# Performance work log

Hardware: AMD Instinct MI355X
Metric: run time of the kernel (lower is better)

The kernel has to match this reference:

```python
import jax, jax.numpy as jnp
import numpy as np

N = 50000   # num nodes
C = 256     # in_channels
O = 256     # out_channels
D = 32      # fixed degree per node
S = 16      # num_samples


def setup_inputs() -> dict:
    key = jax.random.key(0)
    ks = jax.random.split(key, 8)
    w = 1.0 / np.sqrt(C).astype(np.float32)
    x = jax.random.normal(ks[0], (N, C), dtype=jnp.float32)
    neighbors = jax.random.randint(ks[1], (N, D), 0, N)  # padded adjacency (degree D for every node)
    W_self = jax.random.uniform(ks[2], (C, O), dtype=jnp.float32, minval=-w, maxval=w)
    b_self = jax.random.uniform(ks[3], (O,), dtype=jnp.float32, minval=-w, maxval=w)
    W_neigh = jax.random.uniform(ks[4], (C, O), dtype=jnp.float32, minval=-w, maxval=w)
    b_neigh = jax.random.uniform(ks[5], (O,), dtype=jnp.float32, minval=-w, maxval=w)
    W_coarsen = jax.random.uniform(ks[6], (C, O), dtype=jnp.float32, minval=-w, maxval=w)
    b_coarsen = jax.random.uniform(ks[7], (O,), dtype=jnp.float32, minval=-w, maxval=w)
    return dict(x=x, W_self=W_self, b_self=b_self, W_neigh=W_neigh, b_neigh=b_neigh,
                W_coarsen=W_coarsen, b_coarsen=b_coarsen, neighbors=neighbors)


def reference(x, W_self, b_self, W_neigh, b_neigh, W_coarsen, b_coarsen, neighbors):
    # Deterministic partition of each node's D neighbors into S sampled + (D-S) unsampled.
    sampled = neighbors[:, :S]     # [N, S]
    unsampled = neighbors[:, S:]   # [N, D-S]
    # Batched gather + mean aggregation (replaces the per-node Python loop).
    agg_s = jnp.mean(x[sampled], axis=1)    # [N, C]
    agg_u = jnp.mean(x[unsampled], axis=1)  # [N, C]
    # out[v] = W_self x[v] + W_neigh mean(sampled) + W_coarsen mean(unsampled) (+ biases)
    out = (x @ W_self + b_self) + (agg_s @ W_neigh + b_neigh) + (agg_u @ W_coarsen + b_coarsen)
    return out
```

## Files before the change

### kernel.cpp

```cpp
#include <hip/hip_runtime.h>
#include <stdint.h>
#include <stddef.h>


#define NN   50000
#define NPAD 50176
#define ODIM 256
#define NTK  24

typedef __bf16 bf16x8 __attribute__((ext_vector_type(8)));
typedef float  f32x4  __attribute__((ext_vector_type(4)));
typedef float  f32x2  __attribute__((ext_vector_type(2)));
typedef unsigned short u16x8 __attribute__((ext_vector_type(8)));
typedef unsigned short u16x4 __attribute__((ext_vector_type(4)));

static __device__ __forceinline__ unsigned short f2b(float f) {
    unsigned u = __builtin_bit_cast(unsigned, f);
    u += 0x7fffu + ((u >> 16) & 1u);
    return (unsigned short)(u >> 16);
}

__global__ void k_prep_w(const float* __restrict__ Wself, const float* __restrict__ bself,
                         const float* __restrict__ Wneigh, const float* __restrict__ bneigh,
                         const float* __restrict__ Wcoar, const float* __restrict__ bcoar,
                         unsigned short* __restrict__ Wb, float* __restrict__ bias) {
    int k = blockIdx.x;
    int n = threadIdx.x;
    const float* W = (k < 256) ? Wself : (k < 512) ? Wneigh : Wcoar;
    int kl = k & 255;
    float v = W[(size_t)kl * ODIM + n];
    int g = k >> 3;
    int j = k & 7;
    Wb[((size_t)g * ODIM + n) * 8 + j] = f2b(v);
    if (k == 0) bias[n] = bself[n] + bneigh[n] + bcoar[n];
}

__global__ void k_convert_x(const float* __restrict__ x, unsigned short* __restrict__ Ax,
                            unsigned char* __restrict__ X8) {
    int p = blockIdx.x * 256 + threadIdx.x;
    if (p >= NN * 32) return;
    int i  = p >> 5;
    int c8 = p & 31;
    const f32x4* src = (const f32x4*)(x + (size_t)i * 256 + c8 * 8);
    f32x4 v0 = src[0], v1 = src[1];
    u16x8 o;
    o[0] = f2b(v0[0]); o[1] = f2b(v0[1]); o[2] = f2b(v0[2]); o[3] = f2b(v0[3]);
    o[4] = f2b(v1[0]); o[5] = f2b(v1[1]); o[6] = f2b(v1[2]); o[7] = f2b(v1[3]);
    *(u16x8*)(Ax + ((size_t)c8 * NPAD + i) * 8) = o;
    unsigned d0 = __builtin_amdgcn_cvt_pk_fp8_f32(v0[0], v0[1], 0, false);
    d0 = (unsigned)__builtin_amdgcn_cvt_pk_fp8_f32(v0[2], v0[3], d0, true);
    unsigned d1 = __builtin_amdgcn_cvt_pk_fp8_f32(v1[0], v1[1], 0, false);
    d1 = (unsigned)__builtin_amdgcn_cvt_pk_fp8_f32(v1[2], v1[3], d1, true);
    uint2 o8; o8.x = d0; o8.y = d1;
    *(uint2*)(X8 + (size_t)i * 256 + c8 * 8) = o8;
}

__global__ __launch_bounds__(512) void k_gather(const int* __restrict__ nbr,
                                                const unsigned char* __restrict__ X8,
                                                unsigned short* __restrict__ Ax) {
    __shared__ unsigned short aggl[8][512];
    const int wid  = threadIdx.x >> 6;
    const int lane = threadIdx.x & 63;
    const int i = blockIdx.x * 8 + wid;
    const int* nb = nbr + (size_t)i * 32;
    float s0 = 0, s1 = 0, s2 = 0, s3 = 0, u0 = 0, u1 = 0, u2 = 0, u3 = 0;
#pragma unroll
    for (int j = 0; j < 32; ++j) {
        int idx = nb[j];
        unsigned d = *(const unsigned*)(X8 + (size_t)idx * 256 + lane * 4);
        f32x2 lo = __builtin_amdgcn_cvt_pk_f32_fp8(d, false);
        f32x2 hi = __builtin_amdgcn_cvt_pk_f32_fp8(d, true);
        if (j < 16) { s0 += lo[0]; s1 += lo[1]; s2 += hi[0]; s3 += hi[1]; }
        else        { u0 += lo[0]; u1 += lo[1]; u2 += hi[0]; u3 += hi[1]; }
    }
    const float rc = 1.0f / 16.0f;
    u16x4 os = { f2b(s0 * rc), f2b(s1 * rc), f2b(s2 * rc), f2b(s3 * rc) };
    u16x4 ou = { f2b(u0 * rc), f2b(u1 * rc), f2b(u2 * rc), f2b(u3 * rc) };
    *(u16x4*)&aggl[wid][lane * 4]       = os;
    *(u16x4*)&aggl[wid][256 + lane * 4] = ou;
    __syncthreads();
    const int tau = threadIdx.x;
    const int gl = tau >> 3, r = tau & 7;
    u16x8 v = *(const u16x8*)&aggl[r][gl * 8];
    *(u16x8*)(Ax + ((size_t)(32 + gl) * NPAD + blockIdx.x * 8 + r) * 8) = v;
}

__global__ __launch_bounds__(512, 4) void k_gemm(const unsigned short* __restrict__ Ax,
                                                 const unsigned short* __restrict__ Wb,
                                                 const float* __restrict__ bias,
                                                 float* __restrict__ out) {
    __shared__ __align__(16) unsigned short lds[3][12288];
    const int tid  = threadIdx.x;
    const int wid  = tid >> 6;
    const int lane = tid & 63;
    const int l15 = lane & 15, l4 = lane >> 4;
    const int row0 = blockIdx.x * 128;
    const int wr = wid >> 2, wc = wid & 3;

    f32x4 acc[4][4] = {};

    auto stage = [&](int buf, int t) {
#pragma unroll
        for (int i = 0; i < 3; ++i) {
            const int u = wid * 3 + i;
            if (u < 8) {
                const int kc = u >> 1, half = u & 1;
                const int g  = t * 4 + kc;
                const unsigned short* src =
                    Ax + ((size_t)g * NPAD + row0 + half * 64 + lane) * 8;
                unsigned short* dst = &lds[buf][kc * 1024 + half * 512];
                __builtin_amdgcn_global_load_lds(
                    (const __attribute__((address_space(1))) void*)src,
                    (__attribute__((address_space(3))) void*)dst, 16, 0, 0);
            } else {
                const int v = u - 8;
                const int kc = v >> 2, nq = v & 3;
                const int g  = t * 4 + kc;
                const unsigned short* src =
                    Wb + ((size_t)g * ODIM + nq * 64 + lane) * 8;
                unsigned short* dst = &lds[buf][4096 + kc * 2048 + nq * 512];
                __builtin_amdgcn_global_load_lds(
                    (const __attribute__((address_space(1))) void*)src,
                    (__attribute__((address_space(3))) void*)dst, 16, 0, 0);
            }
        }
    };

    stage(0, 0);
    stage(1, 1);
#pragma unroll
    for (int t = 0; t < NTK; ++t) {
        if (t < NTK - 1) asm volatile("s_waitcnt vmcnt(3)" ::: "memory");
        else            asm volatile("s_waitcnt vmcnt(0)" ::: "memory");
        __builtin_amdgcn_s_barrier();
        __builtin_amdgcn_sched_barrier(0);
        if (t + 2 < NTK) stage((t + 2) % 3, t + 2);
        const int buf = t % 3;
        bf16x8 af[4], bfr[4];
#pragma unroll
        for (int mi = 0; mi < 4; ++mi)
            af[mi] = *(const bf16x8*)&lds[buf][l4 * 1024 + (wr * 64 + mi * 16 + l15) * 8];
#pragma unroll
        for (int ni = 0; ni < 4; ++ni)
            bfr[ni] = *(const bf16x8*)&lds[buf][4096 + l4 * 2048 + (wc * 64 + ni * 16 + l15) * 8];
#pragma unroll
        for (int mi = 0; mi < 4; ++mi)
#pragma unroll
            for (int ni = 0; ni < 4; ++ni)
                acc[mi][ni] = __builtin_amdgcn_mfma_f32_16x16x32_bf16(
                    af[mi], bfr[ni], acc[mi][ni], 0, 0, 0);
    }

#pragma unroll
    for (int mi = 0; mi < 4; ++mi) {
        const int row = row0 + wr * 64 + mi * 16 + l4 * 4;
#pragma unroll
        for (int ni = 0; ni < 4; ++ni) {
            const int col = wc * 64 + ni * 16 + l15;
            const float bb = bias[col];
            f32x4 v = acc[mi][ni];
#pragma unroll
            for (int r = 0; r < 4; ++r) {
                const int rr = row + r;
                if (rr < NN) out[(size_t)rr * ODIM + col] = v[r] + bb;
            }
        }
    }
}

extern "C" void kernel_launch(void* const* d_in, const int* in_sizes, int n_in,
                              void* d_out, int out_size, void* d_ws, size_t ws_size,
                              hipStream_t stream) {
    const float* x      = (const float*)d_in[0];
    const float* Wself  = (const float*)d_in[1];
    const float* bself  = (const float*)d_in[2];
    const float* Wneigh = (const float*)d_in[3];
    const float* bneigh = (const float*)d_in[4];
    const float* Wcoar  = (const float*)d_in[5];
    const float* bcoar  = (const float*)d_in[6];
    const int*   nbr    = (const int*)d_in[7];
    float* out = (float*)d_out;

    unsigned short* Ax   = (unsigned short*)d_ws;
    unsigned char*  X8   = (unsigned char*)(Ax + (size_t)96 * NPAD * 8);
    unsigned short* Wb   = (unsigned short*)(X8 + (size_t)NN * 256);
    float*          bias = (float*)(Wb + (size_t)96 * ODIM * 8);

    k_prep_w<<<768, 256, 0, stream>>>(Wself, bself, Wneigh, bneigh, Wcoar, bcoar, Wb, bias);
    k_convert_x<<<(NN * 32 + 255) / 256, 256, 0, stream>>>(x, Ax, X8);
    k_gather<<<NN / 8, 512, 0, stream>>>(nbr, X8, Ax);
    k_gemm<<<NPAD / 128, 512, 0, stream>>>(Ax, Wb, bias, out);
}
```

Before: 105.4 us.

## Split FP8 feature table into channel slabs and gather per slab

The FP8 copy of x is stored as four 64-byte channel slabs, each laid out contiguously over all nodes. The gather kernel now runs a 2D grid where each block handles 16 nodes for one slab, and it stages the neighbor indices in LDS first. The aim is that each slab pass touches a quarter-sized working set (about 3.2 MB), which is more likely to stay in cache during random gathers. The cost is 64-byte gather segments instead of 256-byte ones, and each neighbor list is read four times.

Measured after the change: 98.33 us (median of 2 runs). 1.07x faster.

```diff
diff --git a/kernel.cpp b/kernel.cpp
--- a/kernel.cpp
+++ b/kernel.cpp
@@ -36,7 +36,7 @@
 }
 
 __global__ void k_convert_x(const float* __restrict__ x, unsigned short* __restrict__ Ax,
-                            unsigned char* __restrict__ X8) {
+                            unsigned char* __restrict__ X8s) {
     int p = blockIdx.x * 256 + threadIdx.x;
     if (p >= NN * 32) return;
     int i  = p >> 5;
@@ -52,22 +52,31 @@
     unsigned d1 = __builtin_amdgcn_cvt_pk_fp8_f32(v1[0], v1[1], 0, false);
     d1 = (unsigned)__builtin_amdgcn_cvt_pk_fp8_f32(v1[2], v1[3], d1, true);
     uint2 o8; o8.x = d0; o8.y = d1;
-    *(uint2*)(X8 + (size_t)i * 256 + c8 * 8) = o8;
-}
-
-__global__ __launch_bounds__(512) void k_gather(const int* __restrict__ nbr,
-                                                const unsigned char* __restrict__ X8,
+    const int s = c8 >> 3, b = c8 & 7;
+    *(uint2*)(X8s + ((size_t)s * NN + i) * 64 + b * 8) = o8;
+}
+
+__global__ __launch_bounds__(256) void k_gather(const int* __restrict__ nbr,
+                                                const unsigned char* __restrict__ X8s,
                                                 unsigned short* __restrict__ Ax) {
-    __shared__ unsigned short aggl[8][512];
-    const int wid  = threadIdx.x >> 6;
-    const int lane = threadIdx.x & 63;
-    const int i = blockIdx.x * 8 + wid;
-    const int* nb = nbr + (size_t)i * 32;
+    __shared__ int nbl[512];
+    __shared__ unsigned short aggl[16][136];
+    const int tid   = threadIdx.x;
+    const int node0 = blockIdx.x * 16;
+    const int s     = blockIdx.y;
+    nbl[tid]       = nbr[(size_t)node0 * 32 + tid];
+    nbl[tid + 256] = nbr[(size_t)node0 * 32 + 256 + tid];
+    __syncthreads();
+
+    const int wid = tid >> 6, lane = tid & 63;
+    const int nl  = wid * 4 + (lane >> 4);
+    const int col = lane & 15;
+    const unsigned char* base = X8s + (size_t)s * NN * 64 + col * 4;
     float s0 = 0, s1 = 0, s2 = 0, s3 = 0, u0 = 0, u1 = 0, u2 = 0, u3 = 0;
 #pragma unroll
     for (int j = 0; j < 32; ++j) {
-        int idx = nb[j];
-        unsigned d = *(const unsigned*)(X8 + (size_t)idx * 256 + lane * 4);
+        const int idx = nbl[nl * 32 + j];
+        unsigned d = *(const unsigned*)(base + (size_t)idx * 64);
         f32x2 lo = __builtin_amdgcn_cvt_pk_f32_fp8(d, false);
         f32x2 hi = __builtin_amdgcn_cvt_pk_f32_fp8(d, true);
         if (j < 16) { s0 += lo[0]; s1 += lo[1]; s2 += hi[0]; s3 += hi[1]; }
@@ -76,13 +85,14 @@
     const float rc = 1.0f / 16.0f;
     u16x4 os = { f2b(s0 * rc), f2b(s1 * rc), f2b(s2 * rc), f2b(s3 * rc) };
     u16x4 ou = { f2b(u0 * rc), f2b(u1 * rc), f2b(u2 * rc), f2b(u3 * rc) };
-    *(u16x4*)&aggl[wid][lane * 4]       = os;
-    *(u16x4*)&aggl[wid][256 + lane * 4] = ou;
+    *(u16x4*)&aggl[nl][col * 4]      = os;
+    *(u16x4*)&aggl[nl][64 + col * 4] = ou;
     __syncthreads();
-    const int tau = threadIdx.x;
-    const int gl = tau >> 3, r = tau & 7;
-    u16x8 v = *(const u16x8*)&aggl[r][gl * 8];
-    *(u16x8*)(Ax + ((size_t)(32 + gl) * NPAD + blockIdx.x * 8 + r) * 8) = v;
+
+    const int gch = tid >> 4, row = tid & 15;
+    u16x8 v = *(const u16x8*)&aggl[row][gch * 8];
+    const int g = (gch < 8) ? (32 + s * 8 + gch) : (64 + s * 8 + (gch - 8));
+    *(u16x8*)(Ax + ((size_t)g * NPAD + node0 + row) * 8) = v;
 }
 
 __global__ __launch_bounds__(512, 4) void k_gemm(const unsigned short* __restrict__ Ax,
@@ -182,12 +192,12 @@
     float* out = (float*)d_out;
 
     unsigned short* Ax   = (unsigned short*)d_ws;
-    unsigned char*  X8   = (unsigned char*)(Ax + (size_t)96 * NPAD * 8);
-    unsigned short* Wb   = (unsigned short*)(X8 + (size_t)NN * 256);
+    unsigned char*  X8s  = (unsigned char*)(Ax + (size_t)96 * NPAD * 8);
+    unsigned short* Wb   = (unsigned short*)(X8s + (size_t)4 * NN * 64);
     float*          bias = (float*)(Wb + (size_t)96 * ODIM * 8);
 
     k_prep_w<<<768, 256, 0, stream>>>(Wself, bself, Wneigh, bneigh, Wcoar, bcoar, Wb, bias);
-    k_convert_x<<<(NN * 32 + 255) / 256, 256, 0, stream>>>(x, Ax, X8);
-    k_gather<<<NN / 8, 512, 0, stream>>>(nbr, X8, Ax);
+    k_convert_x<<<(NN * 32 + 255) / 256, 256, 0, stream>>>(x, Ax, X8s);
+    k_gather<<<dim3(3125, 4), 256, 0, stream>>>(nbr, X8s, Ax);
     k_gemm<<<NPAD / 128, 512, 0, stream>>>(Ax, Wb, bias, out);
 }
```

## Split GEMM output columns across blocks and widen gather per-lane loads

Applied to the files above, without the earlier changes.

The GEMM now tiles 128 rows by 128 output columns per block instead of 128x256. That doubles the grid to about 784 blocks, shrinks LDS and accumulators, and raises the occupancy hint to 6 blocks per CU, at the cost of loading each A tile twice. The gather kernel handles 16 nodes per block, stages neighbor indices in shared memory, and has each lane load 8 fp8 bytes at once with half-wave-per-node mapping. The gather also pads the LDS transpose buffer to reduce bank conflicts.

After: 113.0 us. 7.2% more time.

```diff
diff --git a/kernel.cpp b/kernel.cpp
--- a/kernel.cpp
+++ b/kernel.cpp
@@ -58,54 +58,70 @@
 __global__ __launch_bounds__(512) void k_gather(const int* __restrict__ nbr,
                                                 const unsigned char* __restrict__ X8,
                                                 unsigned short* __restrict__ Ax) {
-    __shared__ unsigned short aggl[8][512];
-    const int wid  = threadIdx.x >> 6;
-    const int lane = threadIdx.x & 63;
-    const int i = blockIdx.x * 8 + wid;
-    const int* nb = nbr + (size_t)i * 32;
-    float s0 = 0, s1 = 0, s2 = 0, s3 = 0, u0 = 0, u1 = 0, u2 = 0, u3 = 0;
+    __shared__ int nbl[512];
+    __shared__ unsigned short aggl[16][520];
+    const int tid = threadIdx.x;
+    const int node0 = blockIdx.x * 16;
+    nbl[tid] = nbr[(size_t)node0 * 32 + tid];
+    __syncthreads();
+
+    const int wid = tid >> 6, lane = tid & 63;
+    const int nl  = wid * 2 + (lane >> 5);
+    const int cb  = (lane & 31) * 8;
+    float s0=0,s1=0,s2=0,s3=0,s4=0,s5=0,s6=0,s7=0;
+    float u0=0,u1=0,u2=0,u3=0,u4=0,u5=0,u6=0,u7=0;
 #pragma unroll
     for (int j = 0; j < 32; ++j) {
-        int idx = nb[j];
-        unsigned d = *(const unsigned*)(X8 + (size_t)idx * 256 + lane * 4);
-        f32x2 lo = __builtin_amdgcn_cvt_pk_f32_fp8(d, false);
-        f32x2 hi = __builtin_amdgcn_cvt_pk_f32_fp8(d, true);
-        if (j < 16) { s0 += lo[0]; s1 += lo[1]; s2 += hi[0]; s3 += hi[1]; }
-        else        { u0 += lo[0]; u1 += lo[1]; u2 += hi[0]; u3 += hi[1]; }
+        const int idx = nbl[nl * 32 + j];
+        uint2 d = *(const uint2*)(X8 + (size_t)idx * 256 + cb);
+        f32x2 a0 = __builtin_amdgcn_cvt_pk_f32_fp8(d.x, false);
+        f32x2 a1 = __builtin_amdgcn_cvt_pk_f32_fp8(d.x, true);
+        f32x2 a2 = __builtin_amdgcn_cvt_pk_f32_fp8(d.y, false);
+        f32x2 a3 = __builtin_amdgcn_cvt_pk_f32_fp8(d.y, true);
+        if (j < 16) { s0+=a0[0]; s1+=a0[1]; s2+=a1[0]; s3+=a1[1];
+                      s4+=a2[0]; s5+=a2[1]; s6+=a3[0]; s7+=a3[1]; }
+        else        { u0+=a0[0]; u1+=a0[1]; u2+=a1[0]; u3+=a1[1];
+                      u4+=a2[0]; u5+=a2[1]; u6+=a3[0]; u7+=a3[1]; }
     }
     const float rc = 1.0f / 16.0f;
-    u16x4 os = { f2b(s0 * rc), f2b(s1 * rc), f2b(s2 * rc), f2b(s3 * rc) };
-    u16x4 ou = { f2b(u0 * rc), f2b(u1 * rc), f2b(u2 * rc), f2b(u3 * rc) };
-    *(u16x4*)&aggl[wid][lane * 4]       = os;
-    *(u16x4*)&aggl[wid][256 + lane * 4] = ou;
+    u16x8 os = { f2b(s0*rc), f2b(s1*rc), f2b(s2*rc), f2b(s3*rc),
+                 f2b(s4*rc), f2b(s5*rc), f2b(s6*rc), f2b(s7*rc) };
+    u16x8 ou = { f2b(u0*rc), f2b(u1*rc), f2b(u2*rc), f2b(u3*rc),
+                 f2b(u4*rc), f2b(u5*rc), f2b(u6*rc), f2b(u7*rc) };
+    *(u16x8*)&aggl[nl][cb]       = os;
+    *(u16x8*)&aggl[nl][256 + cb] = ou;
     __syncthreads();
-    const int tau = threadIdx.x;
-    const int gl = tau >> 3, r = tau & 7;
-    u16x8 v = *(const u16x8*)&aggl[r][gl * 8];
-    *(u16x8*)(Ax + ((size_t)(32 + gl) * NPAD + blockIdx.x * 8 + r) * 8) = v;
-}
-
-__global__ __launch_bounds__(512, 4) void k_gemm(const unsigned short* __restrict__ Ax,
+#pragma unroll
+    for (int it = 0; it < 2; ++it) {
+        const int gch = (tid >> 4) + it * 32;
+        const int row = tid & 15;
+        u16x8 v = *(const u16x8*)&aggl[row][gch * 8];
+        *(u16x8*)(Ax + ((size_t)(32 + gch) * NPAD + node0 + row) * 8) = v;
+    }
+}
+
+__global__ __launch_bounds__(512, 6) void k_gemm(const unsigned short* __restrict__ Ax,
                                                  const unsigned short* __restrict__ Wb,
                                                  const float* __restrict__ bias,
                                                  float* __restrict__ out) {
-    __shared__ __align__(16) unsigned short lds[3][12288];
+    __shared__ __align__(16) unsigned short lds[3][8192];
     const int tid  = threadIdx.x;
     const int wid  = tid >> 6;
     const int lane = tid & 63;
     const int l15 = lane & 15, l4 = lane >> 4;
-    const int row0 = blockIdx.x * 128;
-    const int wr = wid >> 2, wc = wid & 3;
-
-    f32x4 acc[4][4] = {};
+    const int row0 = (blockIdx.x >> 1) * 128;
+    const int n0   = (blockIdx.x & 1) * 128;
+    const int wr = wid >> 1, wc = wid & 1;
+
+    f32x4 acc[2][4] = {};
 
     auto stage = [&](int buf, int t) {
 #pragma unroll
-        for (int i = 0; i < 3; ++i) {
-            const int u = wid * 3 + i;
+        for (int i = 0; i < 2; ++i) {
+            const int u = wid * 2 + i;
+            const int kc = (u & 7) >> 1, half = u & 1;
+            const int g  = t * 4 + kc;
             if (u < 8) {
-                const int kc = u >> 1, half = u & 1;
-                const int g  = t * 4 + kc;
                 const unsigned short* src =
                     Ax + ((size_t)g * NPAD + row0 + half * 64 + lane) * 8;
                 unsigned short* dst = &lds[buf][kc * 1024 + half * 512];
@@ -113,12 +129,9 @@
                     (const __attribute__((address_space(1))) void*)src,
                     (__attribute__((address_space(3))) void*)dst, 16, 0, 0);
             } else {
-                const int v = u - 8;
-                const int kc = v >> 2, nq = v & 3;
-                const int g  = t * 4 + kc;
                 const unsigned short* src =
-                    Wb + ((size_t)g * ODIM + nq * 64 + lane) * 8;
-                unsigned short* dst = &lds[buf][4096 + kc * 2048 + nq * 512];
+                    Wb + ((size_t)g * ODIM + n0 + half * 64 + lane) * 8;
+                unsigned short* dst = &lds[buf][4096 + kc * 1024 + half * 512];
                 __builtin_amdgcn_global_load_lds(
                     (const __attribute__((address_space(1))) void*)src,
                     (__attribute__((address_space(3))) void*)dst, 16, 0, 0);
@@ -130,21 +143,21 @@
     stage(1, 1);
 #pragma unroll
     for (int t = 0; t < NTK; ++t) {
-        if (t < NTK - 1) asm volatile("s_waitcnt vmcnt(3)" ::: "memory");
+        if (t < NTK - 1) asm volatile("s_waitcnt vmcnt(2)" ::: "memory");
         else            asm volatile("s_waitcnt vmcnt(0)" ::: "memory");
         __builtin_amdgcn_s_barrier();
         __builtin_amdgcn_sched_barrier(0);
         if (t + 2 < NTK) stage((t + 2) % 3, t + 2);
         const int buf = t % 3;
-        bf16x8 af[4], bfr[4];
-#pragma unroll
-        for (int mi = 0; mi < 4; ++mi)
-            af[mi] = *(const bf16x8*)&lds[buf][l4 * 1024 + (wr * 64 + mi * 16 + l15) * 8];
+        bf16x8 af[2], bfr[4];
+#pragma unroll
+        for (int mi = 0; mi < 2; ++mi)
+            af[mi] = *(const bf16x8*)&lds[buf][l4 * 1024 + (wr * 32 + mi * 16 + l15) * 8];
 #pragma unroll
         for (int ni = 0; ni < 4; ++ni)
-            bfr[ni] = *(const bf16x8*)&lds[buf][4096 + l4 * 2048 + (wc * 64 + ni * 16 + l15) * 8];
-#pragma unroll
-        for (int mi = 0; mi < 4; ++mi)
+            bfr[ni] = *(const bf16x8*)&lds[buf][4096 + l4 * 1024 + (wc * 64 + ni * 16 + l15) * 8];
+#pragma unroll
+        for (int mi = 0; mi < 2; ++mi)
 #pragma unroll
             for (int ni = 0; ni < 4; ++ni)
                 acc[mi][ni] = __builtin_amdgcn_mfma_f32_16x16x32_bf16(
@@ -152,11 +165,11 @@
     }
 
 #pragma unroll
-    for (int mi = 0; mi < 4; ++mi) {
-        const int row = row0 + wr * 64 + mi * 16 + l4 * 4;
+    for (int mi = 0; mi < 2; ++mi) {
+        const int row = row0 + wr * 32 + mi * 16 + l4 * 4;
 #pragma unroll
         for (int ni = 0; ni < 4; ++ni) {
-            const int col = wc * 64 + ni * 16 + l15;
+            const int col = n0 + wc * 64 + ni * 16 + l15;
             const float bb = bias[col];
             f32x4 v = acc[mi][ni];
 #pragma unroll
@@ -188,6 +201,6 @@
 
     k_prep_w<<<768, 256, 0, stream>>>(Wself, bself, Wneigh, bneigh, Wcoar, bcoar, Wb, bias);
     k_convert_x<<<(NN * 32 + 255) / 256, 256, 0, stream>>>(x, Ax, X8);
-    k_gather<<<NN / 8, 512, 0, stream>>>(nbr, X8, Ax);
-    k_gemm<<<NPAD / 128, 512, 0, stream>>>(Ax, Wb, bias, out);
-}
+    k_gather<<<NN / 16, 512, 0, stream>>>(nbr, X8, Ax);
+    k_gemm<<<(NPAD / 128) * 2, 512, 0, stream>>>(Ax, Wb, bias, out);
+}
```
